# Kernel optimization log

Measured on AMD Instinct MI355X. Metric: run time of the kernel, lower is better.

The kernel has to match this reference:

```python
import jax, jax.numpy as jnp
import numpy as np
import math

N_SRC = 100000
N_DST0 = 30000
N_DST1 = 8000
E0 = 200000
E1 = 80000
H, D = 4, 64


def gat_conv(h_src, h_dst, src, dst, W, al, ar, b, n_dst):
    """DGL GATConv (allow_zero_in_degree=True): shared fc, LeakyReLU(0.2), edge softmax."""
    z_src = (h_src @ W).reshape(-1, H, D)              # [Ns,H,D]
    z_dst = (h_dst @ W).reshape(-1, H, D)              # [Nd,H,D]
    el = jnp.sum(z_src * al, axis=-1)                  # [Ns,H]
    er = jnp.sum(z_dst * ar, axis=-1)                  # [Nd,H]
    e = jax.nn.leaky_relu(el[src] + er[dst], 0.2)      # [E,H]
    emax = jax.ops.segment_max(e, dst, num_segments=n_dst)
    emax = jnp.where(jnp.isfinite(emax), emax, 0.0)
    ex = jnp.exp(e - emax[dst])
    denom = jax.ops.segment_sum(ex, dst, num_segments=n_dst)
    denom = jnp.where(denom > 0, denom, 1.0)
    alpha = ex / denom[dst]                            # [E,H]
    out = jax.ops.segment_sum(alpha[:, :, None] * z_src[src], dst, num_segments=n_dst)
    return out + b.reshape(1, H, D)                    # [Nd,H,D]


def attn_pool(feat):
    """Self attention over relation/head slots, then mean over slots (attention(f,f,f).mean(dim=1))."""
    d = feat.shape[-1]
    scores = jnp.einsum('nsd,ntd->nst', feat, feat) / math.sqrt(d)
    p = jax.nn.softmax(scores, axis=-1)
    out = jnp.einsum('nst,ntd->nsd', p, feat)
    return out.mean(axis=1)                            # [N,d]


def rgat_layer(xu, xi, eii, eiu, eui, W, al, ar, b, n_dst_u, n_dst_i):
    du, di = xu[:n_dst_u], xi[:n_dst_i]
    # sorted canonical etypes: ('item','ii','item') < ('item','iu','user') < ('user','ui','item')
    out_ii = gat_conv(xi, di, eii[0], eii[1], W[0], al[0], ar[0], b[0], n_dst_i)
    out_iu = gat_conv(xi, du, eiu[0], eiu[1], W[1], al[1], ar[1], b[1], n_dst_u)
    out_ui = gat_conv(xu, di, eui[0], eui[1], W[2], al[2], ar[2], b[2], n_dst_i)
    feat_u = out_iu                                    # [Nu, H, D]
    feat_i = jnp.concatenate([out_ii, out_ui], axis=1) # [Ni, 2H, D]
    hu = attn_pool(feat_u)
    hi = attn_pool(feat_i)
    return jnp.concatenate([du, hu], axis=1), jnp.concatenate([di, hi], axis=1)


def setup_inputs() -> dict:
    key = jax.random.key(0)
    ks = jax.random.split(key, 24)
    inp = {
        'x_user': jax.random.normal(ks[0], (N_SRC, 64), jnp.float32),
        'x_item': jax.random.normal(ks[1], (N_SRC, 64), jnp.float32),
        'e0_ii_src': jax.random.randint(ks[2], (E0,), 0, N_SRC, jnp.int32),
        'e0_ii_dst': jax.random.randint(ks[3], (E0,), 0, N_DST0, jnp.int32),
        'e0_iu_src': jax.random.randint(ks[4], (E0,), 0, N_SRC, jnp.int32),
        'e0_iu_dst': jax.random.randint(ks[5], (E0,), 0, N_DST0, jnp.int32),
        'e0_ui_src': jax.random.randint(ks[6], (E0,), 0, N_SRC, jnp.int32),
        'e0_ui_dst': jax.random.randint(ks[7], (E0,), 0, N_DST0, jnp.int32),
        'e1_ii_src': jax.random.randint(ks[8], (E1,), 0, N_DST0, jnp.int32),
        'e1_ii_dst': jax.random.randint(ks[9], (E1,), 0, N_DST1, jnp.int32),
        'e1_iu_src': jax.random.randint(ks[10], (E1,), 0, N_DST0, jnp.int32),
        'e1_iu_dst': jax.random.randint(ks[11], (E1,), 0, N_DST1, jnp.int32),
        'e1_ui_src': jax.random.randint(ks[12], (E1,), 0, N_DST0, jnp.int32),
        'e1_ui_dst': jax.random.randint(ks[13], (E1,), 0, N_DST1, jnp.int32),
        'W0': jax.random.normal(ks[14], (3, 64, H * D), jnp.float32) * 0.1,
        'al0': jax.random.normal(ks[15], (3, H, D), jnp.float32) * 0.1,
        'ar0': jax.random.normal(ks[16], (3, H, D), jnp.float32) * 0.1,
        'b0': jnp.zeros((3, H * D), jnp.float32),
        'W1': jax.random.normal(ks[17], (3, 128, H * D), jnp.float32) * 0.1,
        'al1': jax.random.normal(ks[18], (3, H, D), jnp.float32) * 0.1,
        'ar1': jax.random.normal(ks[19], (3, H, D), jnp.float32) * 0.1,
        'b1': jnp.zeros((3, H * D), jnp.float32),
    }
    return inp


def reference(x_user, x_item,
              e0_ii_src, e0_ii_dst, e0_iu_src, e0_iu_dst, e0_ui_src, e0_ui_dst,
              e1_ii_src, e1_ii_dst, e1_iu_src, e1_iu_dst, e1_ui_src, e1_ui_dst,
              W0, al0, ar0, b0, W1, al1, ar1, b1):
    xu, xi = rgat_layer(x_user, x_item,
                        (e0_ii_src, e0_ii_dst), (e0_iu_src, e0_iu_dst), (e0_ui_src, e0_ui_dst),
                        W0, al0, ar0, b0, N_DST0, N_DST0)
    xu, xi = rgat_layer(xu, xi,
                        (e1_ii_src, e1_ii_dst), (e1_iu_src, e1_iu_dst), (e1_ui_src, e1_ui_dst),
                        W1, al1, ar1, b1, N_DST1, N_DST1)
    return jnp.concatenate([xu, xi], axis=0)  # [2*N_DST1, 128+64]
```

## Files before the change

kernel.cpp:

```cpp
#include <hip/hip_runtime.h>

#define NSRC   100000
#define NDST0  30000
#define NDST1  8000
#define E0N    200000
#define E1N    80000
#define HD     256
#define DD     64
#define CAP    64

typedef short bf16x8 __attribute__((ext_vector_type(8)));
typedef float f32x4  __attribute__((ext_vector_type(4)));

static __device__ __forceinline__ unsigned short f2bf(float f) {
    unsigned u = __float_as_uint(f);
    u += 0x7fffu + ((u >> 16) & 1u);
    return (unsigned short)(u >> 16);
}
static __device__ __forceinline__ unsigned pack2(float a, float b) {
    return (unsigned)f2bf(a) | ((unsigned)f2bf(b) << 16);
}
static __device__ __forceinline__ void fma4(float4& a, float s, const float4& b) {
    a.x = fmaf(s, b.x, a.x); a.y = fmaf(s, b.y, a.y);
    a.z = fmaf(s, b.z, a.z); a.w = fmaf(s, b.w, a.w);
}
static __device__ __forceinline__ float dot4(const float4& a, const float4& b) {
    return fmaf(a.x, b.x, fmaf(a.y, b.y, fmaf(a.z, b.z, a.w * b.w)));
}
static __device__ __forceinline__ float4 ld_bf4(const unsigned short* p) {
    uint2 u = *reinterpret_cast<const uint2*>(p);
    float4 r;
    r.x = __uint_as_float(u.x << 16);
    r.y = __uint_as_float(u.x & 0xffff0000u);
    r.z = __uint_as_float(u.y << 16);
    r.w = __uint_as_float(u.y & 0xffff0000u);
    return r;
}
static __device__ __forceinline__ void red4(float4& a, int m) {
    a.x += __shfl_xor(a.x, m, 64);
    a.y += __shfl_xor(a.y, m, 64);
    a.z += __shfl_xor(a.z, m, 64);
    a.w += __shfl_xor(a.w, m, 64);
}

__global__ void k_prep_wlr_all(const float* __restrict__ W, const float* __restrict__ al,
                               const float* __restrict__ ar, float* __restrict__ wl,
                               float* __restrict__ wr, int K)
{
    int tid = blockIdx.x * blockDim.x + threadIdx.x;
    if (tid >= 3 * K * 4) return;
    int r = tid / (K * 4);
    int rem = tid - r * K * 4;
    int k = rem >> 2, h = rem & 3;
    const float* wrow = W + (size_t)r * K * HD + (size_t)k * HD + h * DD;
    const float* a_l = al + r * HD + h * DD;
    const float* a_r = ar + r * HD + h * DD;
    float sl = 0.f, sr = 0.f;
    for (int d = 0; d < DD; ++d) {
        float w = wrow[d];
        sl = fmaf(w, a_l[d], sl);
        sr = fmaf(w, a_r[d], sr);
    }
    wl[r * 512 + k * 4 + h] = sl;
    wr[r * 512 + k * 4 + h] = sr;
}

template<int K, bool TWO>
__global__ __launch_bounds__(256) void k_prep_x(const float* __restrict__ X, int M, int nd,
                                                const float* __restrict__ wlA, const float* __restrict__ wlB,
                                                const float* __restrict__ wrA, const float* __restrict__ wrB,
                                                float* __restrict__ elA, float* __restrict__ elB,
                                                float* __restrict__ erA, float* __restrict__ erB)
{
    int row = blockIdx.x * 256 + threadIdx.x;
    if (row >= M) return;
    const float4* xv = reinterpret_cast<const float4*>(X + (size_t)row * K);
    const float4* wlAv = reinterpret_cast<const float4*>(wlA);
    const float4* wlBv = reinterpret_cast<const float4*>(wlB);
    float4 aA = make_float4(0.f, 0.f, 0.f, 0.f), aB = aA;
    #pragma unroll
    for (int c = 0; c < K / 4; ++c) {
        float4 x4 = xv[c];
        fma4(aA, x4.x, wlAv[c * 4 + 0]); fma4(aA, x4.y, wlAv[c * 4 + 1]);
        fma4(aA, x4.z, wlAv[c * 4 + 2]); fma4(aA, x4.w, wlAv[c * 4 + 3]);
        if (TWO) {
            fma4(aB, x4.x, wlBv[c * 4 + 0]); fma4(aB, x4.y, wlBv[c * 4 + 1]);
            fma4(aB, x4.z, wlBv[c * 4 + 2]); fma4(aB, x4.w, wlBv[c * 4 + 3]);
        }
    }
    *reinterpret_cast<float4*>(elA + (size_t)row * 4) = aA;
    if (TWO) *reinterpret_cast<float4*>(elB + (size_t)row * 4) = aB;
    if (row < nd) {
        const float4* wrAv = reinterpret_cast<const float4*>(wrA);
        const float4* wrBv = reinterpret_cast<const float4*>(wrB);
        float4 rA = make_float4(0.f, 0.f, 0.f, 0.f), rB = rA;
        #pragma unroll
        for (int c = 0; c < K / 4; ++c) {
            float4 x4 = xv[c];
            fma4(rA, x4.x, wrAv[c * 4 + 0]); fma4(rA, x4.y, wrAv[c * 4 + 1]);
            fma4(rA, x4.z, wrAv[c * 4 + 2]); fma4(rA, x4.w, wrAv[c * 4 + 3]);
            if (TWO) {
                fma4(rB, x4.x, wrBv[c * 4 + 0]); fma4(rB, x4.y, wrBv[c * 4 + 1]);
                fma4(rB, x4.z, wrBv[c * 4 + 2]); fma4(rB, x4.w, wrBv[c * 4 + 3]);
            }
        }
        *reinterpret_cast<float4*>(erA + (size_t)row * 4) = rA;
        if (TWO) *reinterpret_cast<float4*>(erB + (size_t)row * 4) = rB;
    }
}

template<int K>
__global__ void k_wt_all(const float* __restrict__ W, unsigned short* __restrict__ Wt)
{
    int r = blockIdx.x;
    const float* Wr = W + (size_t)r * K * HD;
    unsigned short* Wtr = Wt + (size_t)r * 256 * K;
    int c = threadIdx.x;
    #pragma unroll 4
    for (int k = 0; k < K; k += 2) {
        float a = Wr[(size_t)k * HD + c];
        float b = Wr[(size_t)(k + 1) * HD + c];
        *reinterpret_cast<unsigned*>(Wtr + (size_t)c * K + k) = pack2(a, b);
    }
}

__global__ void k_fill3(const int* __restrict__ ed0, const int* __restrict__ ed1,
                        const int* __restrict__ ed2, const int* __restrict__ es0,
                        const int* __restrict__ es1, const int* __restrict__ es2,
                        int* __restrict__ cnt, int* __restrict__ bsrc,
                        int E, int nd, int bpr)
{
    int bx = blockIdx.x;
    int r = (bx >= 2 * bpr) ? 2 : (bx >= bpr ? 1 : 0);
    int e = (bx - r * bpr) * 256 + threadIdx.x;
    if (e >= E) return;
    const int* ed = (r == 0) ? ed0 : (r == 1 ? ed1 : ed2);
    const int* es = (r == 0) ? es0 : (r == 1 ? es1 : es2);
    int d = ed[e];
    int c = atomicAdd(&cnt[(size_t)r * nd + d], 1);
    if (c < CAP) bsrc[((size_t)r * nd + d) * CAP + c] = es[e];
}

template<int K>
__global__ __launch_bounds__(256) void k_agg3(const int* __restrict__ cnt,
                                              const int* __restrict__ bsrc,
                                              const float* __restrict__ el3,
                                              const float* __restrict__ er3,
                                              const float* __restrict__ xsA,
                                              const float* __restrict__ xsB,
                                              unsigned short* __restrict__ aggX,
                                              int nd, int bpr)
{
    constexpr int NV = K / 64;
    int bx = blockIdx.x;
    int r = (bx >= 2 * bpr) ? 2 : (bx >= bpr ? 1 : 0);
    int wid = ((bx - r * bpr) * 256 + (int)threadIdx.x) >> 6;
    int lane = threadIdx.x & 63;
    if (wid >= nd) return;
    int q = lane & 15, g = lane >> 4;
    const float* el = el3 + (size_t)r * NSRC * 4;
    const float* xsrc = (r < 2) ? xsA : xsB;
    int c = cnt[(size_t)r * nd + wid]; if (c > CAP) c = CAP;
    const int* lst = bsrc + ((size_t)r * nd + wid) * CAP;
    float4 er4 = *reinterpret_cast<const float4*>(er3 + (size_t)r * NDST0 * 4 + (size_t)wid * 4);

    int s_own = 0;
    float4 ex_own = make_float4(0.f, 0.f, 0.f, 0.f);
    if (lane < c) {
        s_own = lst[lane];
        float4 e4 = *reinterpret_cast<const float4*>(el + (size_t)s_own * 4);
        e4.x += er4.x; e4.y += er4.y; e4.z += er4.z; e4.w += er4.w;
        e4.x = e4.x > 0.f ? e4.x : 0.2f * e4.x;
        e4.y = e4.y > 0.f ? e4.y : 0.2f * e4.y;
        e4.z = e4.z > 0.f ? e4.z : 0.2f * e4.z;
        e4.w = e4.w > 0.f ? e4.w : 0.2f * e4.w;
        ex_own.x = __expf(e4.x); ex_own.y = __expf(e4.y);
        ex_own.z = __expf(e4.z); ex_own.w = __expf(e4.w);
    }

    float4 acc[4][NV];
    #pragma unroll
    for (int h = 0; h < 4; ++h)
        #pragma unroll
        for (int v = 0; v < NV; ++v) acc[h][v] = make_float4(0.f, 0.f, 0.f, 0.f);
    float4 den = make_float4(0.f, 0.f, 0.f, 0.f);

    const int nt = (c + 3) >> 2;
    for (int t = 0; t < nt; ++t) {
        int i = g + 4 * t;
        int ilane = i & 63;
        int   s   = __shfl(s_own,    ilane, 64);
        float ex0 = __shfl(ex_own.x, ilane, 64);
        float ex1 = __shfl(ex_own.y, ilane, 64);
        float ex2 = __shfl(ex_own.z, ilane, 64);
        float ex3 = __shfl(ex_own.w, ilane, 64);
        if (i < c) {
            const float4* xp = reinterpret_cast<const float4*>(xsrc + (size_t)s * K) + q * NV;
            #pragma unroll
            for (int v = 0; v < NV; ++v) {
                float4 x4 = xp[v];
                fma4(acc[0][v], ex0, x4);
                fma4(acc[1][v], ex1, x4);
                fma4(acc[2][v], ex2, x4);
                fma4(acc[3][v], ex3, x4);
            }
            den.x += ex0; den.y += ex1; den.z += ex2; den.w += ex3;
        }
    }
    #pragma unroll
    for (int m = 16; m < 64; m <<= 1) {
        #pragma unroll
        for (int h = 0; h < 4; ++h)
            #pragma unroll
            for (int v = 0; v < NV; ++v) red4(acc[h][v], m);
        red4(den, m);
    }
    float invh[4];
    invh[0] = den.x > 0.f ? 1.f / den.x : 0.f;
    invh[1] = den.y > 0.f ? 1.f / den.y : 0.f;
    invh[2] = den.z > 0.f ? 1.f / den.z : 0.f;
    invh[3] = den.w > 0.f ? 1.f / den.w : 0.f;
    #pragma unroll
    for (int h = 0; h < 4; ++h) {
        unsigned short* op = aggX + ((size_t)r * nd * 4 + (size_t)wid * 4 + h) * K + q * 4 * NV;
        if (NV == 1) {
            uint2 w;
            w.x = pack2(acc[h][0].x * invh[h], acc[h][0].y * invh[h]);
            w.y = pack2(acc[h][0].z * invh[h], acc[h][0].w * invh[h]);
            *reinterpret_cast<uint2*>(op) = w;
        } else {
            uint4 w;
            w.x = pack2(acc[h][0].x * invh[h], acc[h][0].y * invh[h]);
            w.y = pack2(acc[h][0].z * invh[h], acc[h][0].w * invh[h]);
            w.z = pack2(acc[h][1].x * invh[h], acc[h][1].y * invh[h]);
            w.w = pack2(acc[h][1].z * invh[h], acc[h][1].w * invh[h]);
            *reinterpret_cast<uint4*>(op) = w;
        }
    }
}

template<int K>
__global__ __launch_bounds__(256) void k_gemm3(const unsigned short* __restrict__ aggX,
                                               const unsigned short* __restrict__ Wt3,
                                               unsigned short* __restrict__ outb,
                                               int nd, int bpr)
{
    int bx = blockIdx.x;
    int r = (bx >= 2 * bpr) ? 2 : (bx >= bpr ? 1 : 0);
    const unsigned short* A  = aggX + (size_t)r * nd * 4 * K;
    const unsigned short* Wt = Wt3 + (size_t)r * 256 * K;
    unsigned short* ob = outb + (size_t)r * NDST0 * HD;
    const int lane = threadIdx.x & 63;
    const int wv = threadIdx.x >> 6;
    const int r0 = (bx - r * bpr) * 16;
    const int rr = lane & 15, kg = lane >> 4;
    f32x4 acc[4] = {{0.f,0.f,0.f,0.f},{0.f,0.f,0.f,0.f},{0.f,0.f,0.f,0.f},{0.f,0.f,0.f,0.f}};
    const unsigned short* ap = A + ((size_t)(r0 + rr) * 4 + wv) * K + kg * 8;
    #pragma unroll
    for (int kb = 0; kb < K; kb += 32) {
        bf16x8 a = *reinterpret_cast<const bf16x8*>(ap + kb);
        #pragma unroll
        for (int n = 0; n < 4; ++n) {
            const unsigned short* wp = Wt + (size_t)(wv * 64 + n * 16 + rr) * K + kb + kg * 8;
            bf16x8 b = *reinterpret_cast<const bf16x8*>(wp);
            acc[n] = __builtin_amdgcn_mfma_f32_16x16x32_bf16(a, b, acc[n], 0, 0, 0);
        }
    }
    #pragma unroll
    for (int n = 0; n < 4; ++n)
        #pragma unroll
        for (int i = 0; i < 4; ++i)
            ob[(size_t)(r0 + kg * 4 + i) * HD + wv * 64 + n * 16 + rr] = f2bf(acc[n][i]);
}

template<int S>
__global__ __launch_bounds__(256) void k_pool2(const unsigned short* __restrict__ srcA, const float* __restrict__ bA,
                                               const unsigned short* __restrict__ srcB, const float* __restrict__ bB,
                                               const float* __restrict__ base, int baseCols,
                                               float* __restrict__ dst, int pitch, int colOff, int n)
{
    int wid = (blockIdx.x * 256 + threadIdx.x) >> 6;
    int lane = threadIdx.x & 63;
    int node = wid * 4 + (lane >> 4);
    int q = lane & 15;
    if (node >= n) return;

    float4 f[S];
    #pragma unroll
    for (int s = 0; s < S; ++s) {
        const unsigned short* sp = (s < 4) ? (srcA + (size_t)node * HD + s * DD)
                                           : (srcB + (size_t)node * HD + (s - 4) * DD);
        const float* bp = (s < 4) ? (bA + s * DD) : (bB + (s - 4) * DD);
        float4 v = ld_bf4(sp + q * 4);
        float4 b = *reinterpret_cast<const float4*>(bp + q * 4);
        v.x += b.x; v.y += b.y; v.z += b.z; v.w += b.w;
        f[s] = v;
    }
    constexpr int NE = S * (S + 1) / 2;
    float gt[NE];
    {
        int idx = 0;
        #pragma unroll
        for (int s = 0; s < S; ++s)
            #pragma unroll
            for (int t = s; t < S; ++t)
                gt[idx++] = dot4(f[s], f[t]);
    }
    #pragma unroll
    for (int m = 1; m < 16; m <<= 1) {
        #pragma unroll
        for (int i = 0; i < NE; ++i) gt[i] += __shfl_xor(gt[i], m, 16);
    }
    auto Gv = [&](int s, int t) -> float {
        int a = s < t ? s : t, b2 = s < t ? t : s;
        return gt[a * S - a * (a - 1) / 2 + (b2 - a)];
    };
    float g[S];
    #pragma unroll
    for (int t = 0; t < S; ++t) g[t] = 0.f;
    #pragma unroll
    for (int s = 0; s < S; ++s) {
        float sc[S];
        float m = -1e30f;
        #pragma unroll
        for (int t = 0; t < S; ++t) { sc[t] = Gv(s, t) * 0.125f; m = sc[t] > m ? sc[t] : m; }
        float pe[S];
        float sum = 0.f;
        #pragma unroll
        for (int t = 0; t < S; ++t) { pe[t] = __expf(sc[t] - m); sum += pe[t]; }
        float inv = 1.f / sum;
        #pragma unroll
        for (int t = 0; t < S; ++t) g[t] += pe[t] * inv;
    }
    float4 o = make_float4(0.f, 0.f, 0.f, 0.f);
    #pragma unroll
    for (int t = 0; t < S; ++t) fma4(o, g[t], f[t]);
    const float is = 1.f / S;
    o.x *= is; o.y *= is; o.z *= is; o.w *= is;
    *reinterpret_cast<float4*>(dst + (size_t)node * pitch + colOff + q * 4) = o;
    for (int c = q * 4; c < baseCols; c += 64) {
        float4 v = *reinterpret_cast<const float4*>(base + (size_t)node * baseCols + c);
        *reinterpret_cast<float4*>(dst + (size_t)node * pitch + c) = v;
    }
}

extern "C" void kernel_launch(void* const* d_in, const int* in_sizes, int n_in,
                              void* d_out, int out_size, void* d_ws, size_t ws_size,
                              hipStream_t stream)
{
    const float* x_user = (const float*)d_in[0];
    const float* x_item = (const float*)d_in[1];
    const int* e_s[6] = { (const int*)d_in[2], (const int*)d_in[4], (const int*)d_in[6],
                          (const int*)d_in[8], (const int*)d_in[10], (const int*)d_in[12] };
    const int* e_d[6] = { (const int*)d_in[3], (const int*)d_in[5], (const int*)d_in[7],
                          (const int*)d_in[9], (const int*)d_in[11], (const int*)d_in[13] };
    const float* W0  = (const float*)d_in[14];
    const float* al0 = (const float*)d_in[15];
    const float* ar0 = (const float*)d_in[16];
    const float* b0  = (const float*)d_in[17];
    const float* W1  = (const float*)d_in[18];
    const float* al1 = (const float*)d_in[19];
    const float* ar1 = (const float*)d_in[20];
    const float* b1  = (const float*)d_in[21];
    float* out = (float*)d_out;
    (void)in_sizes; (void)n_in; (void)out_size; (void)ws_size;

    char* p = (char*)d_ws;
    auto take = [&](size_t bytes) { char* r = p; p += (bytes + 255) & ~(size_t)255; return r; };
    unsigned short* out3 = (unsigned short*)take((size_t)3 * NDST0 * HD * 2);
    float* xu1  = (float*)take((size_t)NDST0 * 128 * 4);
    float* xi1  = (float*)take((size_t)NDST0 * 128 * 4);
    unsigned short* aggX = (unsigned short*)take((size_t)3 * NDST0 * 4 * 2 * DD * 2);
    float* el3  = (float*)take((size_t)3 * NSRC * 4 * 4);
    float* er3  = (float*)take((size_t)3 * NDST0 * 4 * 4);
    int*   cntA = (int*)take((size_t)3 * NDST0 * 4);
    int*   cntB = (int*)take((size_t)3 * NDST1 * 4);
    int*   bsrcA = (int*)take((size_t)3 * NDST0 * CAP * 4);
    int*   bsrcB = (int*)take((size_t)3 * NDST1 * CAP * 4);
    unsigned short* Wt3 = (unsigned short*)take((size_t)3 * 256 * 128 * 2);
    float* wl3  = (float*)take((size_t)3 * 512 * 4);
    float* wr3  = (float*)take((size_t)3 * 512 * 4);

    unsigned short* out_ii = out3;
    unsigned short* out_iu = out3 + (size_t)NDST0 * HD;
    unsigned short* out_ui = out3 + (size_t)2 * NDST0 * HD;
    float* el_ii = el3;  float* el_iu = el3 + (size_t)NSRC * 4;  float* el_ui = el3 + (size_t)2 * NSRC * 4;
    float* er_ii = er3;  float* er_iu = er3 + (size_t)NDST0 * 4; float* er_ui = er3 + (size_t)2 * NDST0 * 4;

    hipMemsetAsync(cntA, 0, (size_t)3 * NDST0 * 4, stream);
    hipMemsetAsync(cntB, 0, (size_t)3 * NDST1 * 4, stream);
    {
        const int bpr0 = (E0N + 255) / 256;
        k_fill3<<<3 * bpr0, 256, 0, stream>>>(e_d[0], e_d[1], e_d[2], e_s[0], e_s[1], e_s[2],
                                              cntA, bsrcA, E0N, NDST0, bpr0);
        const int bpr1 = (E1N + 255) / 256;
        k_fill3<<<3 * bpr1, 256, 0, stream>>>(e_d[3], e_d[4], e_d[5], e_s[3], e_s[4], e_s[5],
                                              cntB, bsrcB, E1N, NDST1, bpr1);
    }

    k_prep_wlr_all<<<3, 256, 0, stream>>>(W0, al0, ar0, wl3, wr3, 64);
    k_prep_x<64, true><<<(NSRC + 255) / 256, 256, 0, stream>>>(x_item, NSRC, NDST0,
        wl3, wl3 + 512, wr3, wr3 + 1024, el_ii, el_iu, er_ii, er_ui);
    k_prep_x<64, false><<<(NSRC + 255) / 256, 256, 0, stream>>>(x_user, NSRC, NDST0,
        wl3 + 1024, nullptr, wr3 + 512, nullptr, el_ui, nullptr, er_iu, nullptr);
    k_wt_all<64><<<3, 256, 0, stream>>>(W0, Wt3);

    {
        const int bprA = (NDST0 + 3) / 4;
        k_agg3<64><<<3 * bprA, 256, 0, stream>>>(cntA, bsrcA, el3, er3, x_item, x_user,
                                                 aggX, NDST0, bprA);
        const int bprG = NDST0 / 16;
        k_gemm3<64><<<3 * bprG, 256, 0, stream>>>(aggX, Wt3, out3, NDST0, bprG);
    }
    k_pool2<4><<<NDST0 / 16, 256, 0, stream>>>(out_iu, b0 + 256, out_iu, b0 + 256,
                                               x_user, 64, xu1, 128, 64, NDST0);
    k_pool2<8><<<NDST0 / 16, 256, 0, stream>>>(out_ii, b0, out_ui, b0 + 512,
                                               x_item, 64, xi1, 128, 64, NDST0);

    k_prep_wlr_all<<<6, 256, 0, stream>>>(W1, al1, ar1, wl3, wr3, 128);
    k_prep_x<128, true><<<(NDST0 + 255) / 256, 256, 0, stream>>>(xi1, NDST0, NDST1,
        wl3, wl3 + 512, wr3, wr3 + 1024, el_ii, el_iu, er_ii, er_ui);
    k_prep_x<128, false><<<(NDST0 + 255) / 256, 256, 0, stream>>>(xu1, NDST0, NDST1,
        wl3 + 1024, nullptr, wr3 + 512, nullptr, el_ui, nullptr, er_iu, nullptr);
    k_wt_all<128><<<3, 256, 0, stream>>>(W1, Wt3);

    {
        const int bprA = (NDST1 + 3) / 4;
        k_agg3<128><<<3 * bprA, 256, 0, stream>>>(cntB, bsrcB, el3, er3, xi1, xu1,
                                                  aggX, NDST1, bprA);
        const int bprG = NDST1 / 16;
        k_gemm3<128><<<3 * bprG, 256, 0, stream>>>(aggX, Wt3, out3, NDST1, bprG);
    }
    k_pool2<4><<<NDST1 / 16, 256, 0, stream>>>(out_iu, b1 + 256, out_iu, b1 + 256,
                                               xu1, 128, out, 192, 128, NDST1);
    k_pool2<8><<<NDST1 / 16, 256, 0, stream>>>(out_ii, b1, out_ui, b1 + 512,
                                               xi1, 128, out + (size_t)NDST1 * 192, 192, 128, NDST1);
}
```

Before: 308.8 us.

## Gather bf16 mirrors of source features in aggregation and merge prep kernels

The prep kernel now also writes a bf16 copy of each source feature matrix. The aggregation kernel gathers from that copy instead of fp32, halving the bytes moved by the random per-edge row gathers. The attention-weight and transposed-weight prep kernels are merged into one launch, and the item/user feature prep launches are merged into one, cutting launch count. It costs an extra full write of the bf16 mirrors and rounds the source features to bf16 before aggregation. The aggX scratch buffer is also shrunk.

```diff
diff --git a/kernel.cpp b/kernel.cpp
--- a/kernel.cpp
+++ b/kernel.cpp
@@ -43,84 +43,112 @@
     a.w += __shfl_xor(a.w, m, 64);
 }
 
-__global__ void k_prep_wlr_all(const float* __restrict__ W, const float* __restrict__ al,
-                               const float* __restrict__ ar, float* __restrict__ wl,
-                               float* __restrict__ wr, int K)
-{
-    int tid = blockIdx.x * blockDim.x + threadIdx.x;
-    if (tid >= 3 * K * 4) return;
-    int r = tid / (K * 4);
-    int rem = tid - r * K * 4;
-    int k = rem >> 2, h = rem & 3;
-    const float* wrow = W + (size_t)r * K * HD + (size_t)k * HD + h * DD;
-    const float* a_l = al + r * HD + h * DD;
-    const float* a_r = ar + r * HD + h * DD;
-    float sl = 0.f, sr = 0.f;
-    for (int d = 0; d < DD; ++d) {
-        float w = wrow[d];
-        sl = fmaf(w, a_l[d], sl);
-        sr = fmaf(w, a_r[d], sr);
-    }
-    wl[r * 512 + k * 4 + h] = sl;
-    wr[r * 512 + k * 4 + h] = sr;
-}
-
-template<int K, bool TWO>
-__global__ __launch_bounds__(256) void k_prep_x(const float* __restrict__ X, int M, int nd,
-                                                const float* __restrict__ wlA, const float* __restrict__ wlB,
-                                                const float* __restrict__ wrA, const float* __restrict__ wrB,
-                                                float* __restrict__ elA, float* __restrict__ elB,
-                                                float* __restrict__ erA, float* __restrict__ erB)
-{
-    int row = blockIdx.x * 256 + threadIdx.x;
+template<int K>
+__global__ void k_wprep(const float* __restrict__ W, const float* __restrict__ al,
+                        const float* __restrict__ ar, float* __restrict__ wl,
+                        float* __restrict__ wr, unsigned short* __restrict__ Wt)
+{
+    constexpr int WLRB = (3 * K * 4) / 256;
+    int bx = blockIdx.x;
+    if (bx < WLRB) {
+        int tid = bx * 256 + threadIdx.x;
+        int r = tid / (K * 4);
+        int rem = tid - r * K * 4;
+        int k = rem >> 2, h = rem & 3;
+        const float* wrow = W + (size_t)r * K * HD + (size_t)k * HD + h * DD;
+        const float* a_l = al + r * HD + h * DD;
+        const float* a_r = ar + r * HD + h * DD;
+        float sl = 0.f, sr = 0.f;
+        for (int d = 0; d < DD; ++d) {
+            float w = wrow[d];
+            sl = fmaf(w, a_l[d], sl);
+            sr = fmaf(w, a_r[d], sr);
+        }
+        wl[r * 512 + k * 4 + h] = sl;
+        wr[r * 512 + k * 4 + h] = sr;
+    } else {
+        int r = bx - WLRB;
+        const float* Wr = W + (size_t)r * K * HD;
+        unsigned short* Wtr = Wt + (size_t)r * 256 * K;
+        int c = threadIdx.x;
+        #pragma unroll 4
+        for (int k = 0; k < K; k += 2) {
+            float a = Wr[(size_t)k * HD + c];
+            float b = Wr[(size_t)(k + 1) * HD + c];
+            *reinterpret_cast<unsigned*>(Wtr + (size_t)c * K + k) = pack2(a, b);
+        }
+    }
+}
+
+template<int K, bool MIRROR>
+__global__ __launch_bounds__(256) void k_prep_x2(const float* __restrict__ XA,
+                                                 const float* __restrict__ XB,
+                                                 int M, int nd, int bpr,
+                                                 const float* __restrict__ wl3,
+                                                 const float* __restrict__ wr3,
+                                                 float* __restrict__ el3,
+                                                 float* __restrict__ er3,
+                                                 unsigned short* __restrict__ XbA,
+                                                 unsigned short* __restrict__ XbB)
+{
+    int bx = blockIdx.x;
+    const bool item = bx < bpr;
+    int row = (item ? bx : bx - bpr) * 256 + threadIdx.x;
     if (row >= M) return;
+    const float* X = item ? XA : XB;
     const float4* xv = reinterpret_cast<const float4*>(X + (size_t)row * K);
-    const float4* wlAv = reinterpret_cast<const float4*>(wlA);
-    const float4* wlBv = reinterpret_cast<const float4*>(wlB);
+
+    if (MIRROR) {
+        unsigned short* xbrow = (item ? XbA : XbB) + (size_t)row * K;
+        #pragma unroll
+        for (int c2 = 0; c2 < K / 8; ++c2) {
+            float4 a = xv[2 * c2], b = xv[2 * c2 + 1];
+            uint4 w;
+            w.x = pack2(a.x, a.y); w.y = pack2(a.z, a.w);
+            w.z = pack2(b.x, b.y); w.w = pack2(b.z, b.w);
+            reinterpret_cast<uint4*>(xbrow)[c2] = w;
+        }
+    }
+
+    const float4* wlAv = reinterpret_cast<const float4*>(item ? wl3 : wl3 + 1024);
+    const float4* wlBv = reinterpret_cast<const float4*>(wl3 + 512);
     float4 aA = make_float4(0.f, 0.f, 0.f, 0.f), aB = aA;
     #pragma unroll
     for (int c = 0; c < K / 4; ++c) {
         float4 x4 = xv[c];
         fma4(aA, x4.x, wlAv[c * 4 + 0]); fma4(aA, x4.y, wlAv[c * 4 + 1]);
         fma4(aA, x4.z, wlAv[c * 4 + 2]); fma4(aA, x4.w, wlAv[c * 4 + 3]);
-        if (TWO) {
+        if (item) {
             fma4(aB, x4.x, wlBv[c * 4 + 0]); fma4(aB, x4.y, wlBv[c * 4 + 1]);
             fma4(aB, x4.z, wlBv[c * 4 + 2]); fma4(aB, x4.w, wlBv[c * 4 + 3]);
         }
     }
-    *reinterpret_cast<float4*>(elA + (size_t)row * 4) = aA;
-    if (TWO) *reinterpret_cast<float4*>(elB + (size_t)row * 4) = aB;
+    if (item) {
+        *reinterpret_cast<float4*>(el3 + (size_t)row * 4) = aA;
+        *reinterpret_cast<float4*>(el3 + (size_t)NSRC * 4 + (size_t)row * 4) = aB;
+    } else {
+        *reinterpret_cast<float4*>(el3 + (size_t)2 * NSRC * 4 + (size_t)row * 4) = aA;
+    }
     if (row < nd) {
-        const float4* wrAv = reinterpret_cast<const float4*>(wrA);
-        const float4* wrBv = reinterpret_cast<const float4*>(wrB);
+        const float4* wrAv = reinterpret_cast<const float4*>(item ? wr3 : wr3 + 512);
+        const float4* wrBv = reinterpret_cast<const float4*>(wr3 + 1024);
         float4 rA = make_float4(0.f, 0.f, 0.f, 0.f), rB = rA;
         #pragma unroll
         for (int c = 0; c < K / 4; ++c) {
             float4 x4 = xv[c];
             fma4(rA, x4.x, wrAv[c * 4 + 0]); fma4(rA, x4.y, wrAv[c * 4 + 1]);
             fma4(rA, x4.z, wrAv[c * 4 + 2]); fma4(rA, x4.w, wrAv[c * 4 + 3]);
-            if (TWO) {
+            if (item) {
                 fma4(rB, x4.x, wrBv[c * 4 + 0]); fma4(rB, x4.y, wrBv[c * 4 + 1]);
                 fma4(rB, x4.z, wrBv[c * 4 + 2]); fma4(rB, x4.w, wrBv[c * 4 + 3]);
             }
         }
-        *reinterpret_cast<float4*>(erA + (size_t)row * 4) = rA;
-        if (TWO) *reinterpret_cast<float4*>(erB + (size_t)row * 4) = rB;
-    }
-}
-
-template<int K>
-__global__ void k_wt_all(const float* __restrict__ W, unsigned short* __restrict__ Wt)
-{
-    int r = blockIdx.x;
-    const float* Wr = W + (size_t)r * K * HD;
-    unsigned short* Wtr = Wt + (size_t)r * 256 * K;
-    int c = threadIdx.x;
-    #pragma unroll 4
-    for (int k = 0; k < K; k += 2) {
-        float a = Wr[(size_t)k * HD + c];
-        float b = Wr[(size_t)(k + 1) * HD + c];
-        *reinterpret_cast<unsigned*>(Wtr + (size_t)c * K + k) = pack2(a, b);
+        if (item) {
+            *reinterpret_cast<float4*>(er3 + (size_t)row * 4) = rA;
+            *reinterpret_cast<float4*>(er3 + (size_t)2 * NDST0 * 4 + (size_t)row * 4) = rB;
+        } else {
+            *reinterpret_cast<float4*>(er3 + (size_t)NDST0 * 4 + (size_t)row * 4) = rA;
+        }
     }
 }
 
@@ -146,8 +174,8 @@
                                               const int* __restrict__ bsrc,
                                               const float* __restrict__ el3,
                                               const float* __restrict__ er3,
-                                              const float* __restrict__ xsA,
-                                              const float* __restrict__ xsB,
+                                              const unsigned short* __restrict__ xsA,
+                                              const unsigned short* __restrict__ xsB,
                                               unsigned short* __restrict__ aggX,
                                               int nd, int bpr)
 {
@@ -159,7 +187,7 @@
     if (wid >= nd) return;
     int q = lane & 15, g = lane >> 4;
     const float* el = el3 + (size_t)r * NSRC * 4;
-    const float* xsrc = (r < 2) ? xsA : xsB;
+    const unsigned short* xsrc = (r < 2) ? xsA : xsB;
     int c = cnt[(size_t)r * nd + wid]; if (c > CAP) c = CAP;
     const int* lst = bsrc + ((size_t)r * nd + wid) * CAP;
     float4 er4 = *reinterpret_cast<const float4*>(er3 + (size_t)r * NDST0 * 4 + (size_t)wid * 4);
@@ -195,10 +223,10 @@
         float ex2 = __shfl(ex_own.z, ilane, 64);
         float ex3 = __shfl(ex_own.w, ilane, 64);
         if (i < c) {
-            const float4* xp = reinterpret_cast<const float4*>(xsrc + (size_t)s * K) + q * NV;
+            const unsigned short* xp = xsrc + (size_t)s * K + q * 4 * NV;
             #pragma unroll
             for (int v = 0; v < NV; ++v) {
-                float4 x4 = xp[v];
+                float4 x4 = ld_bf4(xp + v * 4);
                 fma4(acc[0][v], ex0, x4);
                 fma4(acc[1][v], ex1, x4);
                 fma4(acc[2][v], ex2, x4);
@@ -370,7 +398,11 @@
     unsigned short* out3 = (unsigned short*)take((size_t)3 * NDST0 * HD * 2);
     float* xu1  = (float*)take((size_t)NDST0 * 128 * 4);
     float* xi1  = (float*)take((size_t)NDST0 * 128 * 4);
-    unsigned short* aggX = (unsigned short*)take((size_t)3 * NDST0 * 4 * 2 * DD * 2);
+    unsigned short* xib  = (unsigned short*)take((size_t)NSRC * DD * 2);
+    unsigned short* xub  = (unsigned short*)take((size_t)NSRC * DD * 2);
+    unsigned short* xi1b = (unsigned short*)take((size_t)NDST0 * 128 * 2);
+    unsigned short* xu1b = (unsigned short*)take((size_t)NDST0 * 128 * 2);
+    unsigned short* aggX = (unsigned short*)take((size_t)3 * NDST0 * 4 * DD * 2);
     float* el3  = (float*)take((size_t)3 * NSRC * 4 * 4);
     float* er3  = (float*)take((size_t)3 * NDST0 * 4 * 4);
     int*   cntA = (int*)take((size_t)3 * NDST0 * 4);
@@ -384,8 +416,6 @@
     unsigned short* out_ii = out3;
     unsigned short* out_iu = out3 + (size_t)NDST0 * HD;
     unsigned short* out_ui = out3 + (size_t)2 * NDST0 * HD;
-    float* el_ii = el3;  float* el_iu = el3 + (size_t)NSRC * 4;  float* el_ui = el3 + (size_t)2 * NSRC * 4;
-    float* er_ii = er3;  float* er_iu = er3 + (size_t)NDST0 * 4; float* er_ui = er3 + (size_t)2 * NDST0 * 4;
 
     hipMemsetAsync(cntA, 0, (size_t)3 * NDST0 * 4, stream);
     hipMemsetAsync(cntB, 0, (size_t)3 * NDST1 * 4, stream);
@@ -398,16 +428,15 @@
                                               cntB, bsrcB, E1N, NDST1, bpr1);
     }
 
-    k_prep_wlr_all<<<3, 256, 0, stream>>>(W0, al0, ar0, wl3, wr3, 64);
-    k_prep_x<64, true><<<(NSRC + 255) / 256, 256, 0, stream>>>(x_item, NSRC, NDST0,
-        wl3, wl3 + 512, wr3, wr3 + 1024, el_ii, el_iu, er_ii, er_ui);
-    k_prep_x<64, false><<<(NSRC + 255) / 256, 256, 0, stream>>>(x_user, NSRC, NDST0,
-        wl3 + 1024, nullptr, wr3 + 512, nullptr, el_ui, nullptr, er_iu, nullptr);
-    k_wt_all<64><<<3, 256, 0, stream>>>(W0, Wt3);
-
+    k_wprep<64><<<6, 256, 0, stream>>>(W0, al0, ar0, wl3, wr3, Wt3);
+    {
+        const int bpr = (NSRC + 255) / 256;
+        k_prep_x2<64, true><<<2 * bpr, 256, 0, stream>>>(x_item, x_user, NSRC, NDST0, bpr,
+                                                         wl3, wr3, el3, er3, xib, xub);
+    }
     {
         const int bprA = (NDST0 + 3) / 4;
-        k_agg3<64><<<3 * bprA, 256, 0, stream>>>(cntA, bsrcA, el3, er3, x_item, x_user,
+        k_agg3<64><<<3 * bprA, 256, 0, stream>>>(cntA, bsrcA, el3, er3, xib, xub,
                                                  aggX, NDST0, bprA);
         const int bprG = NDST0 / 16;
         k_gemm3<64><<<3 * bprG, 256, 0, stream>>>(aggX, Wt3, out3, NDST0, bprG);
@@ -417,16 +446,15 @@
     k_pool2<8><<<NDST0 / 16, 256, 0, stream>>>(out_ii, b0, out_ui, b0 + 512,
                                                x_item, 64, xi1, 128, 64, NDST0);
 
-    k_prep_wlr_all<<<6, 256, 0, stream>>>(W1, al1, ar1, wl3, wr3, 128);
-    k_prep_x<128, true><<<(NDST0 + 255) / 256, 256, 0, stream>>>(xi1, NDST0, NDST1,
-        wl3, wl3 + 512, wr3, wr3 + 1024, el_ii, el_iu, er_ii, er_ui);
-    k_prep_x<128, false><<<(NDST0 + 255) / 256, 256, 0, stream>>>(xu1, NDST0, NDST1,
-        wl3 + 1024, nullptr, wr3 + 512, nullptr, el_ui, nullptr, er_iu, nullptr);
-    k_wt_all<128><<<3, 256, 0, stream>>>(W1, Wt3);
-
+    k_wprep<128><<<9, 256, 0, stream>>>(W1, al1, ar1, wl3, wr3, Wt3);
+    {
+        const int bpr = (NDST0 + 255) / 256;
+        k_prep_x2<128, true><<<2 * bpr, 256, 0, stream>>>(xi1, xu1, NDST0, NDST1, bpr,
+                                                          wl3, wr3, el3, er3, xi1b, xu1b);
+    }
     {
         const int bprA = (NDST1 + 3) / 4;
-        k_agg3<128><<<3 * bprA, 256, 0, stream>>>(cntB, bsrcB, el3, er3, xi1, xu1,
+        k_agg3<128><<<3 * bprA, 256, 0, stream>>>(cntB, bsrcB, el3, er3, xi1b, xu1b,
                                                   aggX, NDST1, bprA);
         const int bprG = NDST1 / 16;
         k_gemm3<128><<<3 * bprG, 256, 0, stream>>>(aggX, Wt3, out3, NDST1, bprG);
```

Measured after the change: 345.6 us. 11.9% more time.
